# Optimization experiments

Hardware: AMD Instinct MI355X
Metric: run time of the kernel (lower is better)

## Reference

```python
import jax, jax.numpy as jnp
import numpy as np

B, S, D, F, R = 4, 2048, 2048, 8192, 16


def setup_inputs() -> dict:
    key = jax.random.key(0)
    ks = jax.random.split(key, 13)
    sc = 0.02  # weight scale to keep activations well-conditioned
    return {
        "x1": jax.random.normal(ks[0], (B, S, D), jnp.float32),
        "w_gate": jax.random.normal(ks[1], (D, F), jnp.float32) * sc,
        "b_gate": jax.random.normal(ks[2], (F,), jnp.float32) * sc,
        "w_gate_lora_a": jax.random.normal(ks[3], (D, R), jnp.float32) * sc,
        "w_gate_lora_b": jax.random.normal(ks[4], (R, F), jnp.float32) * sc,
        "w_up": jax.random.normal(ks[5], (D, F), jnp.float32) * sc,
        "b_up": jax.random.normal(ks[6], (F,), jnp.float32) * sc,
        "w_up_lora_a": jax.random.normal(ks[7], (D, R), jnp.float32) * sc,
        "w_up_lora_b": jax.random.normal(ks[8], (R, F), jnp.float32) * sc,
        "w_down": jax.random.normal(ks[9], (F, D), jnp.float32) * sc,
        "b_down": jax.random.normal(ks[10], (D,), jnp.float32) * sc,
        "w_down_lora_a": jax.random.normal(ks[11], (F, R), jnp.float32) * sc,
        "w_down_lora_b": jax.random.normal(ks[12], (R, D), jnp.float32) * sc,
    }


def reference(x1, w_gate, b_gate, w_gate_lora_a, w_gate_lora_b,
              w_up, b_up, w_up_lora_a, w_up_lora_b,
              w_down, b_down, w_down_lora_a, w_down_lora_b):
    # gate projection: dequantized base GEMM + bias + rank-R LoRA
    y1 = x1 @ w_gate + b_gate + (x1 @ w_gate_lora_a) @ w_gate_lora_b  # [B,S,F]
    # up projection
    y2 = x1 @ w_up + b_up + (x1 @ w_up_lora_a) @ w_up_lora_b          # [B,S,F]
    # activation_forward == 'relu' gated product
    x3 = jax.nn.relu(y1) * y2                                          # [B,S,F]
    # down projection
    y3 = x3 @ w_down + b_down + (x3 @ w_down_lora_a) @ w_down_lora_b  # [B,S,D]
    return y3
```

## Files before the change

kernel.cpp:

```cpp
#include <hip/hip_runtime.h>

typedef __bf16 bf16x8 __attribute__((ext_vector_type(8)));
typedef float f32x4 __attribute__((ext_vector_type(4)));

#define MFMA16(a, b, c) __builtin_amdgcn_mfma_f32_16x16x32_bf16((a), (b), (c), 0, 0, 0)

__device__ __forceinline__ unsigned short f2bf(float f) {
    unsigned int u = __float_as_uint(f);
    u += 0x7fffu + ((u >> 16) & 1u);
    return (unsigned short)(u >> 16);
}

__device__ __forceinline__ void gload16(const unsigned short* g, unsigned short* l) {
    __builtin_amdgcn_global_load_lds(
        (__attribute__((address_space(1))) void*)(void*)g,
        (__attribute__((address_space(3))) void*)(void*)l,
        16, 0, 0);
}


__device__ __forceinline__ void ld_frag4(const unsigned short* base, int w0, int h,
                                         int l16, int quad, bf16x8* f) {
#pragma unroll
    for (int i = 0; i < 4; ++i) {
        const int r = w0 + i * 16 + l16;
        f[i] = *(const bf16x8*)(base + r * 64 + (((h * 4 + quad) ^ (r & 7)) * 8));
    }
}

__device__ __forceinline__ void mfma16x(const bf16x8* af, const bf16x8* bf, f32x4 (*acc)[4]) {
    __builtin_amdgcn_s_setprio(1);
#pragma unroll
    for (int i = 0; i < 4; ++i)
#pragma unroll
        for (int j = 0; j < 4; ++j) acc[i][j] = MFMA16(af[i], bf[j], acc[i][j]);
    __builtin_amdgcn_s_setprio(0);
}

#define ASM_VMCNT6 asm volatile("s_waitcnt vmcnt(6)" ::: "memory")
#define ASM_VMCNT2 asm volatile("s_waitcnt vmcnt(2)" ::: "memory")
#define ASM_VMCNT0 asm volatile("s_waitcnt vmcnt(0)" ::: "memory")
#define ASM_LGKM0  asm volatile("s_waitcnt lgkmcnt(0)" ::: "memory")

__global__ void cast_x_kernel(const float4* __restrict__ x, ushort4* __restrict__ xb) {
    const size_t i = (size_t)blockIdx.x * 256 + threadIdx.x;
    const float4 v = x[i];
    ushort4 o;
    o.x = f2bf(v.x); o.y = f2bf(v.y); o.z = f2bf(v.z); o.w = f2bf(v.w);
    xb[i] = o;
}

__global__ void prep_wT(const float* __restrict__ W, const float* __restrict__ A,
                        const float* __restrict__ B2, unsigned short* __restrict__ WT,
                        const int K, const int N) {
    __shared__ float tile[64][65];
    __shared__ float As[64][16];
    __shared__ float Bs[16][64];
    const int t = threadIdx.x;
    const int k0 = blockIdx.x * 64;
    const int n0 = blockIdx.y * 64;

    for (int i = t; i < 64 * 16; i += 256)
        As[i >> 4][i & 15] = A[(size_t)(k0 + (i >> 4)) * 16 + (i & 15)];
    for (int i = t; i < 16 * 64; i += 256)
        Bs[i >> 6][i & 63] = B2[(size_t)(i >> 6) * N + n0 + (i & 63)];
    __syncthreads();

    const int c = t & 63;
    const int r0 = t >> 6;
    for (int rr = 0; rr < 64; rr += 4) {
        const int r = rr + r0;
        float v = W[(size_t)(k0 + r) * N + n0 + c];
#pragma unroll
        for (int q = 0; q < 16; ++q) v += As[r][q] * Bs[q][c];
        tile[r][c] = v;
    }
    __syncthreads();
    for (int rr = 0; rr < 64; rr += 4) {
        const int r = rr + r0;
        WT[(size_t)(n0 + r) * K + k0 + c] = f2bf(tile[c][r]);
    }
}

__global__ __launch_bounds__(512, 2)
void gemm_gateup(const unsigned short* __restrict__ Xb,
                 const unsigned short* __restrict__ WgT,
                 const unsigned short* __restrict__ WuT,
                 const float* __restrict__ bg, const float* __restrict__ bu,
                 unsigned short* __restrict__ X3) {
    constexpr int K = 2048, F = 8192, BK = 64, NT = K / BK;
    extern __shared__ __align__(16) unsigned short lds[];
    unsigned short* const A0 = lds;
    unsigned short* const G0 = lds + 32768;
    unsigned short* const U0 = lds + 49152;

    const int tid = threadIdx.x;
    const int lane = tid & 63;
    const int wave = tid >> 6;
    const int wm = (wave >> 1) * 64;
    const int wn = (wave & 1) * 64;
    const int l16 = lane & 15;
    const int quad = lane >> 4;

    const int m0 = blockIdx.x * 256;
    const int n0 = blockIdx.y * 128;

    const unsigned short* Ag = Xb + (size_t)m0 * K;
    const unsigned short* Gg = WgT + (size_t)n0 * K;
    const unsigned short* Ug = WuT + (size_t)n0 * K;

    int srow[2], soff[2];
#pragma unroll
    for (int j = 0; j < 2; ++j) {
        const int c = tid + j * 512;
        srow[j] = c >> 3;
        soff[j] = ((c & 7) ^ (srow[j] & 7)) * 8;
    }
    const int dst0 = tid * 8, dst1 = (tid + 512) * 8;

#define STAGE(gptr, lbase, kk, roff)                                                        \
    do {                                                                                    \
        gload16((gptr) + (size_t)(srow[0] + (roff)) * K + (kk) + soff[0], (lbase) + dst0);  \
        gload16((gptr) + (size_t)(srow[1] + (roff)) * K + (kk) + soff[1], (lbase) + dst1);  \
    } while (0)

    f32x4 accg[4][4] = {};
    f32x4 accu[4][4] = {};
    bf16x8 af[4], bfr[4];

    STAGE(Ag, A0, 0, 0);
    STAGE(Ag, A0 + 8192, 0, 128);
    STAGE(Gg, G0, 0, 0);
    STAGE(Ug, U0, 0, 0);
    ASM_VMCNT2;
    __builtin_amdgcn_s_barrier();
    __builtin_amdgcn_sched_barrier(0);

    for (int t = 0; t < NT; ++t) {
        const int p = t & 1, q = p ^ 1;
        const unsigned short* Ap = A0 + p * 16384;
        const unsigned short* Gp = G0 + p * 8192;
        const unsigned short* Up = U0 + p * 8192;
        unsigned short* const Aq = A0 + q * 16384;
        unsigned short* const Gq = G0 + q * 8192;
        unsigned short* const Uq = U0 + q * 8192;
        const int kn = (t + 1) * BK;
        const bool pf = (t + 1 < NT);

        ld_frag4(Ap, wm, 0, l16, quad, af);
        ld_frag4(Gp, wn, 0, l16, quad, bfr);
        if (pf) STAGE(Ag, Aq, kn, 0);
        __builtin_amdgcn_s_barrier();
        ASM_LGKM0;
        __builtin_amdgcn_sched_barrier(0);
        mfma16x(af, bfr, accg);
        if (pf) {
            ASM_VMCNT2;
        } else {
            ASM_VMCNT0;
        }
        __builtin_amdgcn_s_barrier();
        __builtin_amdgcn_sched_barrier(0);

        ld_frag4(Up, wn, 0, l16, quad, bfr);
        if (pf) STAGE(Ag, Aq + 8192, kn, 128);
        __builtin_amdgcn_s_barrier();
        ASM_LGKM0;
        __builtin_amdgcn_sched_barrier(0);
        mfma16x(af, bfr, accu);
        __builtin_amdgcn_s_barrier();

        ld_frag4(Ap, wm, 1, l16, quad, af);
        ld_frag4(Gp, wn, 1, l16, quad, bfr);
        if (pf) STAGE(Gg, Gq, kn, 0);
        __builtin_amdgcn_s_barrier();
        ASM_LGKM0;
        __builtin_amdgcn_sched_barrier(0);
        mfma16x(af, bfr, accg);
        __builtin_amdgcn_s_barrier();

        ld_frag4(Up, wn, 1, l16, quad, bfr);
        if (pf) STAGE(Ug, Uq, kn, 0);
        __builtin_amdgcn_s_barrier();
        ASM_LGKM0;
        __builtin_amdgcn_sched_barrier(0);
        mfma16x(af, bfr, accu);
        ASM_VMCNT2;
        __builtin_amdgcn_s_barrier();
        __builtin_amdgcn_sched_barrier(0);
    }
#undef STAGE

#pragma unroll
    for (int j = 0; j < 4; ++j) {
        const int col = n0 + wn + j * 16 + l16;
        const float bgv = bg[col];
        const float buv = bu[col];
#pragma unroll
        for (int i = 0; i < 4; ++i) {
            const int rowb = m0 + wm + i * 16 + quad * 4;
#pragma unroll
            for (int r = 0; r < 4; ++r) {
                float g = accg[i][j][r] + bgv;
                float u = accu[i][j][r] + buv;
                g = g > 0.f ? g : 0.f;
                X3[(size_t)(rowb + r) * F + col] = f2bf(g * u);
            }
        }
    }
}

__global__ __launch_bounds__(512, 2)
void gemm_down(const unsigned short* __restrict__ X3,
               const unsigned short* __restrict__ WdT,
               const float* __restrict__ bd, float* __restrict__ out) {
    constexpr int K = 8192, N = 2048, BK = 64, NT = K / BK;
    extern __shared__ __align__(16) unsigned short lds[];
#define ABUF(b) (lds + (b) * 24576)
#define BBUF(b) (lds + (b) * 24576 + 16384)

    const int tid = threadIdx.x;
    const int lane = tid & 63;
    const int wave = tid >> 6;
    const int wm = (wave >> 1) * 64;
    const int wn = (wave & 1) * 64;
    const int l16 = lane & 15;
    const int quad = lane >> 4;

    const int m0 = blockIdx.x * 256;
    const int n0 = blockIdx.y * 128;

    const unsigned short* Ag = X3 + (size_t)m0 * K;
    const unsigned short* Bg = WdT + (size_t)n0 * K;

    int srow[2], soff[2];
#pragma unroll
    for (int j = 0; j < 2; ++j) {
        const int c = tid + j * 512;
        srow[j] = c >> 3;
        soff[j] = ((c & 7) ^ (srow[j] & 7)) * 8;
    }
    const int dst0 = tid * 8, dst1 = (tid + 512) * 8;

#define STAGE(gptr, lbase, kk, roff)                                                        \
    do {                                                                                    \
        gload16((gptr) + (size_t)(srow[0] + (roff)) * K + (kk) + soff[0], (lbase) + dst0);  \
        gload16((gptr) + (size_t)(srow[1] + (roff)) * K + (kk) + soff[1], (lbase) + dst1);  \
    } while (0)

    f32x4 acc[4][4] = {};
    bf16x8 af[4], bfr[4];

    STAGE(Ag, ABUF(0), 0, 0);
    STAGE(Ag, ABUF(0) + 8192, 0, 128);
    STAGE(Bg, BBUF(0), 0, 0);
    STAGE(Ag, ABUF(1), BK, 0);
    STAGE(Ag, ABUF(1) + 8192, BK, 128);
    STAGE(Bg, BBUF(1), BK, 0);
    ASM_VMCNT6;
    __builtin_amdgcn_s_barrier();
    __builtin_amdgcn_sched_barrier(0);

    for (int t = 0; t < NT; ++t) {
        const unsigned short* Ap = ABUF(t % 3);
        const unsigned short* Bp = BBUF(t % 3);
        const int qb = (t + 2) % 3;
        const int kn = (t + 2) * BK;
        const bool pf = (t + 2 < NT);

        ld_frag4(Ap, wm, 0, l16, quad, af);
        ld_frag4(Bp, wn, 0, l16, quad, bfr);
        if (pf) {
            STAGE(Ag, ABUF(qb), kn, 0);
            STAGE(Ag, ABUF(qb) + 8192, kn, 128);
        }
        __builtin_amdgcn_s_barrier();
        ASM_LGKM0;
        __builtin_amdgcn_sched_barrier(0);
        mfma16x(af, bfr, acc);
        __builtin_amdgcn_s_barrier();

        ld_frag4(Ap, wm, 1, l16, quad, af);
        ld_frag4(Bp, wn, 1, l16, quad, bfr);
        if (pf) STAGE(Bg, BBUF(qb), kn, 0);
        __builtin_amdgcn_s_barrier();
        ASM_LGKM0;
        __builtin_amdgcn_sched_barrier(0);
        mfma16x(af, bfr, acc);
        if (pf) {
            ASM_VMCNT6;
        } else {
            ASM_VMCNT0;
        }
        __builtin_amdgcn_s_barrier();
        __builtin_amdgcn_sched_barrier(0);
    }
#undef STAGE
#undef ABUF
#undef BBUF

#pragma unroll
    for (int j = 0; j < 4; ++j) {
        const int col = n0 + wn + j * 16 + l16;
        const float bdv = bd[col];
#pragma unroll
        for (int i = 0; i < 4; ++i) {
            const int rowb = m0 + wm + i * 16 + quad * 4;
#pragma unroll
            for (int r = 0; r < 4; ++r)
                out[(size_t)(rowb + r) * N + col] = acc[i][j][r] + bdv;
        }
    }
}

extern "C" void kernel_launch(void* const* d_in, const int* in_sizes, int n_in,
                              void* d_out, int out_size, void* d_ws, size_t ws_size,
                              hipStream_t stream) {
    const float* x1      = (const float*)d_in[0];
    const float* w_gate  = (const float*)d_in[1];
    const float* b_gate  = (const float*)d_in[2];
    const float* a_gate  = (const float*)d_in[3];
    const float* lb_gate = (const float*)d_in[4];
    const float* w_up    = (const float*)d_in[5];
    const float* b_up    = (const float*)d_in[6];
    const float* a_up    = (const float*)d_in[7];
    const float* lb_up   = (const float*)d_in[8];
    const float* w_down  = (const float*)d_in[9];
    const float* b_down  = (const float*)d_in[10];
    const float* a_down  = (const float*)d_in[11];
    const float* lb_down = (const float*)d_in[12];

    constexpr int M = 8192, D = 2048, F = 8192;

    static bool attr_set = false;
    if (!attr_set) {
        (void)hipFuncSetAttribute((const void*)gemm_gateup,
                                  hipFuncAttributeMaxDynamicSharedMemorySize, 131072);
        (void)hipFuncSetAttribute((const void*)gemm_down,
                                  hipFuncAttributeMaxDynamicSharedMemorySize, 147456);
        attr_set = true;
    }

    char* ws = (char*)d_ws;
    unsigned short* Xb  = (unsigned short*)ws;
    unsigned short* WgT = (unsigned short*)(ws + 33554432ULL);
    unsigned short* WuT = (unsigned short*)(ws + 67108864ULL);
    unsigned short* WdT = (unsigned short*)(ws + 100663296ULL);
    unsigned short* X3  = (unsigned short*)(ws + 134217728ULL);

    cast_x_kernel<<<dim3((M * D) / 4 / 256), dim3(256), 0, stream>>>(
        (const float4*)x1, (ushort4*)Xb);
    prep_wT<<<dim3(D / 64, F / 64), dim3(256), 0, stream>>>(w_gate, a_gate, lb_gate, WgT, D, F);
    prep_wT<<<dim3(D / 64, F / 64), dim3(256), 0, stream>>>(w_up, a_up, lb_up, WuT, D, F);
    prep_wT<<<dim3(F / 64, D / 64), dim3(256), 0, stream>>>(w_down, a_down, lb_down, WdT, F, D);

    gemm_gateup<<<dim3(M / 256, F / 128), dim3(512), 131072, stream>>>(
        Xb, WgT, WuT, b_gate, b_up, X3);
    gemm_down<<<dim3(M / 256, D / 128), dim3(512), 147456, stream>>>(
        X3, WdT, b_down, (float*)d_out);
}
```

Baseline: 1.011 ms.

## Drop redundant workgroup barriers in GEMM loops and vectorize weight prep kernel

Removes most of the s_barrier calls between the LDS-fragment-load and MFMA phases in the gate/up and down GEMM main loops. Only the barriers that follow the vmcnt waits are kept, so waves are held together less often. Separately, it rewrites prep_wT so each thread handles four columns with float4 loads, a vectorized LoRA merge and ushort4 stores. The barrier removal cuts synchronization stalls but makes the reuse of double- and triple-buffered LDS depend on the remaining barriers, which risks races if a wave races ahead.

```diff
diff --git a/kernel.cpp b/kernel.cpp
--- a/kernel.cpp
+++ b/kernel.cpp
@@ -41,6 +41,8 @@
 #define ASM_VMCNT2 asm volatile("s_waitcnt vmcnt(2)" ::: "memory")
 #define ASM_VMCNT0 asm volatile("s_waitcnt vmcnt(0)" ::: "memory")
 #define ASM_LGKM0  asm volatile("s_waitcnt lgkmcnt(0)" ::: "memory")
+#define SBAR __builtin_amdgcn_s_barrier()
+#define SCHED0 __builtin_amdgcn_sched_barrier(0)
 
 __global__ void cast_x_kernel(const float4* __restrict__ x, ushort4* __restrict__ xb) {
     const size_t i = (size_t)blockIdx.x * 256 + threadIdx.x;
@@ -60,25 +62,36 @@
     const int k0 = blockIdx.x * 64;
     const int n0 = blockIdx.y * 64;
 
-    for (int i = t; i < 64 * 16; i += 256)
-        As[i >> 4][i & 15] = A[(size_t)(k0 + (i >> 4)) * 16 + (i & 15)];
-    for (int i = t; i < 16 * 64; i += 256)
-        Bs[i >> 6][i & 63] = B2[(size_t)(i >> 6) * N + n0 + (i & 63)];
+    {
+        const int ar = t >> 2, aq = (t & 3) * 4;
+        *(float4*)&As[ar][aq] = *(const float4*)&A[(size_t)(k0 + ar) * 16 + aq];
+        const int br = t >> 4, bc = (t & 15) * 4;
+        *(float4*)&Bs[br][bc] = *(const float4*)&B2[(size_t)br * N + n0 + bc];
+    }
     __syncthreads();
 
-    const int c = t & 63;
-    const int r0 = t >> 6;
-    for (int rr = 0; rr < 64; rr += 4) {
+    const int c4 = (t & 15) * 4;
+    const int r0 = t >> 4;
+    for (int rr = 0; rr < 64; rr += 16) {
         const int r = rr + r0;
-        float v = W[(size_t)(k0 + r) * N + n0 + c];
-#pragma unroll
-        for (int q = 0; q < 16; ++q) v += As[r][q] * Bs[q][c];
-        tile[r][c] = v;
+        float4 v = *(const float4*)&W[(size_t)(k0 + r) * N + n0 + c4];
+#pragma unroll
+        for (int q = 0; q < 16; ++q) {
+            const float a = As[r][q];
+            v.x += a * Bs[q][c4];     v.y += a * Bs[q][c4 + 1];
+            v.z += a * Bs[q][c4 + 2]; v.w += a * Bs[q][c4 + 3];
+        }
+        tile[r][c4] = v.x; tile[r][c4 + 1] = v.y;
+        tile[r][c4 + 2] = v.z; tile[r][c4 + 3] = v.w;
     }
     __syncthreads();
-    for (int rr = 0; rr < 64; rr += 4) {
+
+    for (int rr = 0; rr < 64; rr += 16) {
         const int r = rr + r0;
-        WT[(size_t)(n0 + r) * K + k0 + c] = f2bf(tile[c][r]);
+        ushort4 o;
+        o.x = f2bf(tile[c4][r]);     o.y = f2bf(tile[c4 + 1][r]);
+        o.z = f2bf(tile[c4 + 2][r]); o.w = f2bf(tile[c4 + 3][r]);
+        *(ushort4*)&WT[(size_t)(n0 + r) * K + k0 + c4] = o;
     }
 }
 
@@ -133,8 +146,8 @@
     STAGE(Gg, G0, 0, 0);
     STAGE(Ug, U0, 0, 0);
     ASM_VMCNT2;
-    __builtin_amdgcn_s_barrier();
-    __builtin_amdgcn_sched_barrier(0);
+    SBAR;
+    SCHED0;
 
     for (int t = 0; t < NT; ++t) {
         const int p = t & 1, q = p ^ 1;
@@ -150,44 +163,38 @@
         ld_frag4(Ap, wm, 0, l16, quad, af);
         ld_frag4(Gp, wn, 0, l16, quad, bfr);
         if (pf) STAGE(Ag, Aq, kn, 0);
-        __builtin_amdgcn_s_barrier();
-        ASM_LGKM0;
-        __builtin_amdgcn_sched_barrier(0);
+        ASM_LGKM0;
+        SCHED0;
         mfma16x(af, bfr, accg);
         if (pf) {
             ASM_VMCNT2;
         } else {
             ASM_VMCNT0;
         }
-        __builtin_amdgcn_s_barrier();
-        __builtin_amdgcn_sched_barrier(0);
+        SBAR;
+        SCHED0;
 
         ld_frag4(Up, wn, 0, l16, quad, bfr);
         if (pf) STAGE(Ag, Aq + 8192, kn, 128);
-        __builtin_amdgcn_s_barrier();
-        ASM_LGKM0;
-        __builtin_amdgcn_sched_barrier(0);
+        ASM_LGKM0;
+        SCHED0;
         mfma16x(af, bfr, accu);
-        __builtin_amdgcn_s_barrier();
 
         ld_frag4(Ap, wm, 1, l16, quad, af);
         ld_frag4(Gp, wn, 1, l16, quad, bfr);
         if (pf) STAGE(Gg, Gq, kn, 0);
-        __builtin_amdgcn_s_barrier();
-        ASM_LGKM0;
-        __builtin_amdgcn_sched_barrier(0);
+        ASM_LGKM0;
+        SCHED0;
         mfma16x(af, bfr, accg);
-        __builtin_amdgcn_s_barrier();
 
         ld_frag4(Up, wn, 1, l16, quad, bfr);
         if (pf) STAGE(Ug, Uq, kn, 0);
-        __builtin_amdgcn_s_barrier();
-        ASM_LGKM0;
-        __builtin_amdgcn_sched_barrier(0);
+        ASM_LGKM0;
+        SCHED0;
         mfma16x(af, bfr, accu);
         ASM_VMCNT2;
-        __builtin_amdgcn_s_barrier();
-        __builtin_amdgcn_sched_barrier(0);
+        SBAR;
+        SCHED0;
     }
 #undef STAGE
 
@@ -258,8 +265,8 @@
     STAGE(Ag, ABUF(1) + 8192, BK, 128);
     STAGE(Bg, BBUF(1), BK, 0);
     ASM_VMCNT6;
-    __builtin_amdgcn_s_barrier();
-    __builtin_amdgcn_sched_barrier(0);
+    SBAR;
+    SCHED0;
 
     for (int t = 0; t < NT; ++t) {
         const unsigned short* Ap = ABUF(t % 3);
@@ -274,26 +281,23 @@
             STAGE(Ag, ABUF(qb), kn, 0);
             STAGE(Ag, ABUF(qb) + 8192, kn, 128);
         }
-        __builtin_amdgcn_s_barrier();
-        ASM_LGKM0;
-        __builtin_amdgcn_sched_barrier(0);
+        ASM_LGKM0;
+        SCHED0;
         mfma16x(af, bfr, acc);
-        __builtin_amdgcn_s_barrier();
 
         ld_frag4(Ap, wm, 1, l16, quad, af);
         ld_frag4(Bp, wn, 1, l16, quad, bfr);
         if (pf) STAGE(Bg, BBUF(qb), kn, 0);
-        __builtin_amdgcn_s_barrier();
-        ASM_LGKM0;
-        __builtin_amdgcn_sched_barrier(0);
+        ASM_LGKM0;
+        SCHED0;
         mfma16x(af, bfr, acc);
         if (pf) {
             ASM_VMCNT6;
         } else {
             ASM_VMCNT0;
         }
-        __builtin_amdgcn_s_barrier();
-        __builtin_amdgcn_sched_barrier(0);
+        SBAR;
+        SCHED0;
     }
 #undef STAGE
 #undef ABUF
```

After: 965.1 us. -4.6%, faster.
